# Kernel tuning notes

Hardware: AMD Instinct MI355X
Metric: run time of the kernel (lower is better)

Reference implementation:

```python
import math
import jax
import jax.numpy as jnp
import numpy as np

B = 4
SEQ_LEN = 512
ENC_IN = 21
TIME_DIM = 4
D_MODEL = 256
N_HEADS = 8
HEAD_DIM = D_MODEL // N_HEADS  # 32
NUM_K = 4
PATCH_LEN = 16
STRIDE = 8
EFF_LEN = (SEQ_LEN - PATCH_LEN) // STRIDE + 1  # 63, pad_len == 0
D_FF = 1024
PRED_LEN = 96
N_NEW = 2
N_ENC = 2
EPS = 1e-5


def setup_inputs() -> dict:
    key = jax.random.key(0)
    ks = iter(jax.random.split(key, 100))
    def nrm(shape, s=1.0):
        return jax.random.normal(next(ks), shape, jnp.float32) * s
    H, Dh, T, K = N_HEADS, HEAD_DIM, TIME_DIM, NUM_K
    inp = {}
    inp['x_enc'] = nrm((B, SEQ_LEN, ENC_IN))
    inp['x_mark_enc'] = jax.random.uniform(next(ks), (B, SEQ_LEN, TIME_DIM), jnp.float32)
    inp['x_dec'] = nrm((B, 144, ENC_IN))
    inp['x_mark_dec'] = jax.random.uniform(next(ks), (B, 144, TIME_DIM), jnp.float32)
    # DataEmbedding2: token conv (circular, k=3, no bias); positional enc is computed analytically
    inp['tok_W'] = nrm((D_MODEL, ENC_IN, 3), 0.05)
    # PatchEmbedding conv
    inp['patch_W'] = nrm((D_MODEL, D_MODEL, PATCH_LEN), 0.02)
    inp['patch_b'] = jnp.zeros((D_MODEL,), jnp.float32)
    # TimeKernelAttentionA layers (stacked on leading axis)
    inp['nl_WQ'] = nrm((N_NEW, D_MODEL, D_MODEL), 0.05)
    inp['nl_WK'] = nrm((N_NEW, D_MODEL, D_MODEL), 0.05)
    inp['nl_WV'] = nrm((N_NEW, D_MODEL, D_MODEL), 0.05)
    inp['nl_WO'] = nrm((N_NEW, D_MODEL, D_MODEL), 0.05)
    inp['nl_bO'] = jnp.zeros((N_NEW, D_MODEL), jnp.float32)
    inp['nl_mu_abs'] = nrm((N_NEW, H, Dh, T, K))
    inp['nl_sigma_abs'] = jnp.abs(nrm((N_NEW, H, Dh, T, K))) + 0.5
    inp['nl_w_abs'] = nrm((N_NEW, H, Dh, T, K), 0.1)
    inp['nl_mu_rel'] = nrm((N_NEW, H, Dh, T, K))
    inp['nl_sigma_rel'] = jnp.abs(nrm((N_NEW, H, Dh, T, K))) + 0.5
    inp['nl_w_rel'] = nrm((N_NEW, H, Dh, T, K), 0.1)
    inp['nl_alpha'] = jnp.ones((N_NEW, H), jnp.float32)
    inp['nl_beta'] = jnp.ones((N_NEW, H), jnp.float32)
    inp['nl_gamma'] = jnp.zeros((N_NEW, H), jnp.float32)
    # DataEmbedding_inverted: Linear(EFF_LEN -> d_model)
    inp['inv_W'] = nrm((D_MODEL, EFF_LEN), 0.05)
    inp['inv_b'] = jnp.zeros((D_MODEL,), jnp.float32)
    # Encoder layers (stacked)
    inp['el_Wq'] = nrm((N_ENC, D_MODEL, D_MODEL), 0.05)
    inp['el_bq'] = jnp.zeros((N_ENC, D_MODEL), jnp.float32)
    inp['el_Wk'] = nrm((N_ENC, D_MODEL, D_MODEL), 0.05)
    inp['el_bk'] = jnp.zeros((N_ENC, D_MODEL), jnp.float32)
    inp['el_Wv'] = nrm((N_ENC, D_MODEL, D_MODEL), 0.05)
    inp['el_bv'] = jnp.zeros((N_ENC, D_MODEL), jnp.float32)
    inp['el_Wo'] = nrm((N_ENC, D_MODEL, D_MODEL), 0.05)
    inp['el_bo'] = jnp.zeros((N_ENC, D_MODEL), jnp.float32)
    inp['el_W1'] = nrm((N_ENC, D_FF, D_MODEL), 0.05)
    inp['el_b1'] = jnp.zeros((N_ENC, D_FF), jnp.float32)
    inp['el_W2'] = nrm((N_ENC, D_MODEL, D_FF), 0.05)
    inp['el_b2'] = jnp.zeros((N_ENC, D_MODEL), jnp.float32)
    inp['el_n1_g'] = jnp.ones((N_ENC, D_MODEL), jnp.float32)
    inp['el_n1_b'] = jnp.zeros((N_ENC, D_MODEL), jnp.float32)
    inp['el_n2_g'] = jnp.ones((N_ENC, D_MODEL), jnp.float32)
    inp['el_n2_b'] = jnp.zeros((N_ENC, D_MODEL), jnp.float32)
    inp['norm_g'] = jnp.ones((D_MODEL,), jnp.float32)
    inp['norm_b'] = jnp.zeros((D_MODEL,), jnp.float32)
    inp['proj_W'] = nrm((PRED_LEN, D_MODEL), 0.05)
    inp['proj_b'] = jnp.zeros((PRED_LEN,), jnp.float32)
    return inp


def _conv1d(x, w, stride):
    # x: [B, Cin, L], w: [Cout, Cin, k]
    return jax.lax.conv_general_dilated(x, w, (stride,), 'VALID', dimension_numbers=('NCH', 'OIH', 'NCH'))


def _ln(x, g, b):
    m = x.mean(-1, keepdims=True)
    v = jnp.var(x, axis=-1, keepdims=True)
    return (x - m) / jnp.sqrt(v + EPS) * g + b


def _gauss(t, mu, sigma, w):
    # t: [B, N, T]; mu/sigma/w: [H, D, T, K] -> [B, H, D, N] (sum over T, K)
    diff = t[:, None, None, :, :, None] - mu[None, :, :, None, :, :]
    g = w[None, :, :, None, :, :] * jnp.exp(-(diff * diff) / (2.0 * sigma[None, :, :, None, :, :] ** 2))
    return g.sum((-1, -2))


def _tka(x, t, WQ, WK, WV, WO, bO, mu_a, sg_a, w_a, mu_r, sg_r, w_r, alpha, beta, gamma):
    Bn, L, _ = x.shape
    H, Dh = N_HEADS, HEAD_DIM
    q = (x @ WQ.T).reshape(Bn, L, H, Dh).transpose(0, 2, 1, 3)
    k = (x @ WK.T).reshape(Bn, L, H, Dh).transpose(0, 2, 1, 3)
    v = (x @ WV.T).reshape(Bn, L, H, Dh).transpose(0, 2, 1, 3)
    Xh = x.reshape(Bn, L, H, Dh).transpose(0, 2, 1, 3)
    Pij = jnp.einsum('bhid,bhjd->bhij', Xh, Xh)
    g_abs = _gauss(t, mu_a, sg_a, w_a)  # [B,H,D,L]
    t_rel = jnp.abs(t[:, :, None, :] - t[:, None, :, :]).reshape(Bn, L * L, TIME_DIM)
    g_rel = _gauss(t_rel, mu_r, sg_r, w_r).reshape(Bn, H, Dh, L, L).mean(2)  # [B,H,L,L]
    gi = g_abs.mean(2)  # [B,H,L]
    # NOTE: in the original, g_abs_j = g_abs_i.unsqueeze(-1).expand(...,L) (constant over j),
    # so (g_abs_i.unsqueeze(-1) + g_abs_j) == 2 * g_abs_i broadcast over j. We preserve that.
    a = alpha[None, :, None, None]
    b = beta[None, :, None, None]
    c = gamma[None, :, None, None]
    A = a * Pij * (2.0 * gi[..., None]) + b * Pij * g_rel + c
    scores = jnp.einsum('bhid,bhjd->bhij', q, k) / math.sqrt(Dh) * A
    attn = jax.nn.softmax(scores, axis=-1)
    out = jnp.einsum('bhij,bhjd->bhid', attn, v).transpose(0, 2, 1, 3).reshape(Bn, L, D_MODEL)
    return out @ WO.T + bO


def reference(x_enc, x_mark_enc, x_dec, x_mark_dec, tok_W, patch_W, patch_b, nl_WQ, nl_WK, nl_WV, nl_WO, nl_bO, nl_mu_abs, nl_sigma_abs, nl_w_abs, nl_mu_rel, nl_sigma_rel, nl_w_rel, nl_alpha, nl_beta, nl_gamma, inv_W, inv_b, el_Wq, el_bq, el_Wk, el_bk, el_Wv, el_bv, el_Wo, el_bo, el_W1, el_b1, el_W2, el_b2, el_n1_g, el_n1_b, el_n2_g, el_n2_b, norm_g, norm_b, proj_W, proj_b):
    # --- instance normalization (use_norm) ---
    means = x_enc.mean(1, keepdims=True)
    x = x_enc - means
    stdev = jnp.sqrt(jnp.var(x, axis=1, keepdims=True) + EPS)
    x = x / stdev
    # --- DataEmbedding2: TokenEmbedding (circular conv k=3) + sinusoidal PE, x_mark=None ---
    xc = x.transpose(0, 2, 1)  # [B, C, L]
    xp = jnp.concatenate([xc[:, :, -1:], xc, xc[:, :, :1]], axis=2)  # circular pad 1
    val = _conv1d(xp, tok_W, 1).transpose(0, 2, 1)  # [B, L, d]
    pos = jnp.arange(SEQ_LEN, dtype=jnp.float32)[:, None]
    div = jnp.exp(jnp.arange(0, D_MODEL, 2, dtype=jnp.float32) * (-math.log(10000.0) / D_MODEL))
    pe = jnp.zeros((SEQ_LEN, D_MODEL), jnp.float32)
    pe = pe.at[:, 0::2].set(jnp.sin(pos * div)).at[:, 1::2].set(jnp.cos(pos * div))
    enc = val + pe[None]
    # --- PatchEmbedding (pad_len == 0 for these dims) ---
    enc = _conv1d(enc.transpose(0, 2, 1), patch_W, STRIDE).transpose(0, 2, 1) + patch_b  # [B, 63, d]
    idx = jnp.arange(EFF_LEN)[:, None] * STRIDE + jnp.arange(PATCH_LEN)[None, :]
    t = x_mark_enc[:, idx, :].mean(2)  # [B, 63, T] (unfold + mean)
    # --- TimeKernelAttentionA stack ---
    for i in range(N_NEW):
        enc = _tka(enc, t, nl_WQ[i], nl_WK[i], nl_WV[i], nl_WO[i], nl_bO[i], nl_mu_abs[i], nl_sigma_abs[i], nl_w_abs[i], nl_mu_rel[i], nl_sigma_rel[i], nl_w_rel[i], nl_alpha[i], nl_beta[i], nl_gamma[i])
    # --- DataEmbedding_inverted ---
    xi = jnp.concatenate([enc.transpose(0, 2, 1), t.transpose(0, 2, 1)], axis=1)  # [B, d+T, 63]
    enc = xi @ inv_W.T + inv_b  # [B, d+T, d]
    # --- Encoder (FullAttention + FFN) ---
    Bn, Nt, _ = enc.shape
    for i in range(N_ENC):
        q = (enc @ el_Wq[i].T + el_bq[i]).reshape(Bn, Nt, N_HEADS, HEAD_DIM)
        k = (enc @ el_Wk[i].T + el_bk[i]).reshape(Bn, Nt, N_HEADS, HEAD_DIM)
        v = (enc @ el_Wv[i].T + el_bv[i]).reshape(Bn, Nt, N_HEADS, HEAD_DIM)
        sc = jnp.einsum('blhe,bshe->bhls', q, k) / math.sqrt(HEAD_DIM)
        attn = jax.nn.softmax(sc, axis=-1)
        o = jnp.einsum('bhls,bshd->blhd', attn, v).reshape(Bn, Nt, D_MODEL)
        o = o @ el_Wo[i].T + el_bo[i]
        xn = _ln(enc + o, el_n1_g[i], el_n1_b[i])
        y = jax.nn.gelu(xn @ el_W1[i].T + el_b1[i], approximate=False)
        y = y @ el_W2[i].T + el_b2[i]
        enc = _ln(xn + y, el_n2_g[i], el_n2_b[i])
    enc = _ln(enc, norm_g, norm_b)
    # --- projector + de-normalization ---
    dec = (enc @ proj_W.T + proj_b).transpose(0, 2, 1)[:, :, :ENC_IN]  # [B, pred_len, N]
    dec = dec * stdev[:, 0, :][:, None, :] + means[:, 0, :][:, None, :]
    return dec[:, -PRED_LEN:, :]
```

## Files before the change

### kernel.cpp

```cpp
#include <hip/hip_runtime.h>
#include <hip/hip_bf16.h>

#define NB 4
#define SEQ 512
#define CIN 21
#define TDIM 4
#define DM 256
#define NH 8
#define PLEN 16
#define PSTR 8
#define EL 63
#define DFF 1024
#define PRED 96
#define NT 260
#define EPSV 1e-5f

#define T_nlWQ 0
#define T_nlWK 131072
#define T_nlWV 262144
#define T_nlWO 393216
#define T_elWq 524288
#define T_elWk 655360
#define T_elWv 786432
#define T_elWo 917504
// ... 9 lines not shown
  float s1 = v, s2 = v * v;
  #pragma unroll
  for (int off = 32; off > 0; off >>= 1) {
    s1 += __shfl_down(s1, off, 64);
    s2 += __shfl_down(s2, off, 64);
  }
  int wid = threadIdx.x >> 6, lane = threadIdx.x & 63;
  if (lane == 0) { sb[wid * 2] = s1; sb[wid * 2 + 1] = s2; }
  __syncthreads();
  float m = (sb[0] + sb[2] + sb[4] + sb[6]) * (1.0f / 256.0f);
  float q = (sb[1] + sb[3] + sb[5] + sb[7]) * (1.0f / 256.0f);
  return make_float2(m, q - m * m);
}

__device__ __forceinline__ void load16f(const float* p, float* o) {
  const float4* q = reinterpret_cast<const float4*>(p);
  float4 a = q[0], b = q[1], c = q[2], d = q[3];
  o[0]=a.x; o[1]=a.y; o[2]=a.z; o[3]=a.w;
  o[4]=b.x; o[5]=b.y; o[6]=b.z; o[7]=b.w;
  o[8]=c.x; o[9]=c.y; o[10]=c.z; o[11]=c.w;
  o[12]=d.x; o[13]=d.y; o[14]=d.z; o[15]=d.w;
}

__device__ __forceinline__ float dot32(const float4* a, const float4* b) {
  float s = 0.f;
  #pragma unroll
  for (int i = 0; i < 8; ++i) {
    float4 x = a[i], y = b[i];
    s += x.x*y.x + x.y*y.y + x.z*y.z + x.w*y.w;
  }
  return s;
}

__global__ void __launch_bounds__(256) k_wT(
    const float* __restrict__ nlWQ, const float* __restrict__ nlWK,
    const float* __restrict__ nlWV, const float* __restrict__ nlWO,
    const float* __restrict__ eWq, const float* __restrict__ eWk,
    const float* __restrict__ eWv, const float* __restrict__ eWo,
    const float* __restrict__ eW1, const float* __restrict__ eW2,
    const float* __restrict__ invW, const float* __restrict__ projW,
    const float* __restrict__ tokW, const float* __restrict__ patW,
    float* __restrict__ wt) {
  int blk = blockIdx.x;
  const float* src; float* dst; int R, C, tr, tc;
  if (blk < 1024) {
    int m = blk >> 6, tile = blk & 63;
    tr = tile >> 3; tc = tile & 7; R = 256; C = 256;
    int p = m >> 1, l = m & 1;
    const float* bases[8] = {nlWQ, nlWK, nlWV, nlWO, eWq, eWk, eWv, eWo};
    const int offs[8] = {T_nlWQ, T_nlWK, T_nlWV, T_nlWO, T_elWq, T_elWk, T_elWv, T_elWo};
    src = bases[p] + l * 65536;
    dst = wt + offs[p] + l * 65536;
  } else if (blk < 1536) {
    int q = blk - 1024; int l = q >> 8, s = q & 255;
    tr = s >> 3; tc = s & 7; R = 1024; C = 256;
    src = eW1 + l * 262144; dst = wt + T_elW1 + l * 262144;
  } else if (blk < 2048) {
    int q = blk - 1536; int l = q >> 8, s = q & 255;
    tr = s >> 5; tc = s & 31; R = 256; C = 1024;
    src = eW2 + l * 262144; dst = wt + T_elW2 + l * 262144;
  } else if (blk < 3072) {
    int q = blk - 2048; tr = q >> 7; tc = q & 127; R = 256; C = 4096;
    src = patW; dst = wt + T_pat;
  } else if (blk < 3088) {
    int q = blk - 3072; tr = q >> 1; tc = q & 1; R = 256; C = 63;
    src = invW; dst = wt + T_inv;
  } else if (blk < 3112) {
    int q = blk - 3088; tr = q >> 3; tc = q & 7; R = 96; C = 256;
    src = projW; dst = wt + T_proj;
  } else {
    int q = blk - 3112; tr = q >> 1; tc = q & 1; R = 256; C = 63;
    src = tokW; dst = wt + T_tok;
  }
  __shared__ float ts[32][33];
  int tx = threadIdx.x & 31, ty = threadIdx.x >> 5;
  #pragma unroll
  for (int i = 0; i < 4; ++i) {
    int r = tr * 32 + ty + i * 8, c = tc * 32 + tx;
    ts[ty + i * 8][tx] = (c < C) ? src[(size_t)r * C + c] : 0.f;
  }
  __syncthreads();
  #pragma unroll
  for (int i = 0; i < 4; ++i) {
    int c = tc * 32 + ty + i * 8, r = tr * 32 + tx;
    if (c < C) dst[(size_t)c * R + r] = ts[tx][ty + i * 8];
  }
}

__global__ void k_stats(const float* __restrict__ x, const float* __restrict__ xm,
                        float* __restrict__ means, float* __restrict__ stdev,
                        float* __restrict__ tout) {
  int blk = blockIdx.x;
  int t = threadIdx.x;
  if (blk < NB * CIN) {
    int b = blk / CIN, c = blk % CIN;
    const float* p = x + (size_t)b * SEQ * CIN + c;
    float v0 = p[t * CIN];
    float v1 = p[(t + 256) * CIN];
    float s1 = v0 + v1, s2 = v0 * v0 + v1 * v1;
    __shared__ float sb[8];
    #pragma unroll
    for (int off = 32; off > 0; off >>= 1) {
      s1 += __shfl_down(s1, off, 64);
      s2 += __shfl_down(s2, off, 64);
    }
    int wid = t >> 6, lane = t & 63;
    if (lane == 0) { sb[wid * 2] = s1; sb[wid * 2 + 1] = s2; }
    __syncthreads();
    if (t == 0) {
      float a = sb[0] + sb[2] + sb[4] + sb[6];
      float q = sb[1] + sb[3] + sb[5] + sb[7];
      float m = a * (1.0f / 512.0f);
      float var = q * (1.0f / 512.0f) - m * m;
      means[blk] = m;
      stdev[blk] = sqrtf(var + EPSV);
    }
  } else {
    int idx = (blk - NB * CIN) * 256 + t;
    if (idx >= NB * EL * TDIM) return;
    int b = idx / (EL * TDIM), r = idx % (EL * TDIM);
    int l = r >> 2, ti = r & 3;
    const float* p = xm + (size_t)b * SEQ * TDIM + (size_t)l * PSTR * TDIM + ti;
    float s = 0.f;
    #pragma unroll
    for (int k = 0; k < PLEN; ++k) s += p[k * TDIM];
    tout[idx] = s * (1.f / 16.f);
  }
}

__global__ void __launch_bounds__(256) k_tokconv(
    const float* __restrict__ x, const float* __restrict__ tokWT,
    const float* __restrict__ means, const float* __restrict__ stdev,
    float* __restrict__ enc1) {
  int bi = blockIdx.x;
  int b = bi >> 6, sg = bi & 63;
  int s0 = sg * 8;
  __shared__ float sxr[10 * CIN];
  int t = threadIdx.x;
  if (t < 10 * CIN) {
    int li = t / CIN, c = t % CIN;
    int row = (s0 - 1 + li + SEQ) & 511;
    sxr[t] = (x[(size_t)b * SEQ * CIN + row * CIN + c] - means[b * CIN + c])
             / stdev[b * CIN + c];
  }
  __syncthreads();
  int d = t;
  float wreg[63];
  #pragma unroll
  for (int q = 0; q < 63; ++q) wreg[q] = tokWT[q * DM + d];
  int de = d & ~1;
  float dv = expf((float)de * (-9.210340371976184f / 256.0f));
  bool isodd = (d & 1);
  #pragma unroll 1
  for (int k = 0; k < 8; ++k) {
    float acc = 0.f;
    const float* sr = sxr + k * CIN;
    #pragma unroll
    for (int c = 0; c < CIN; ++c) {
      acc += sr[c]           * wreg[c * 3 + 0];
// ... 167 lines not shown
    for (int q = 0; q < 4; ++q)
      #pragma unroll
      for (int r = 0; r < 8; ++r) {
        float xv = xb[r * DM + k0 + q];
        acc[r][0] += xv * w[q].x; acc[r][1] += xv * w[q].y;
        acc[r][2] += xv * w[q].z; acc[r][3] += xv * w[q].w;
      }
  }
  if (kq) {
    #pragma unroll
    for (int r = 0; r < 8; ++r)
      reinterpret_cast<float4*>(sp)[((kq - 1) * 8 + r) * 64 + colg] =
          make_float4(acc[r][0], acc[r][1], acc[r][2], acc[r][3]);
  }
  __syncthreads();
  if (kq == 0) {
    float4 b4 = reinterpret_cast<const float4*>(bias)[colg];
    const float4* sp4 = reinterpret_cast<const float4*>(sp);
    #pragma unroll
    for (int r = 0; r < 8; ++r) {
      float4 p0 = sp4[(0 * 8 + r) * 64 + colg];
      float4 p1 = sp4[(1 * 8 + r) * 64 + colg];
      float4 p2 = sp4[(2 * 8 + r) * 64 + colg];
      float4 o;
      o.x = acc[r][0] + p0.x + p1.x + p2.x + b4.x;
      o.y = acc[r][1] + p0.y + p1.y + p2.y + b4.y;
      o.z = acc[r][2] + p0.z + p1.z + p2.z + b4.z;
      o.w = acc[r][3] + p0.w + p1.w + p2.w + b4.w;
      reinterpret_cast<float4*>(out + (size_t)(row0 + r) * DM)[colg] = o;
    }
  }
}

__global__ void __launch_bounds__(256) k_grel2(
    const float* __restrict__ tws,
    const float* __restrict__ mu_r, const float* __restrict__ sg_r,
    const float* __restrict__ w_r,
    const float* __restrict__ mu_a, const float* __restrict__ sg_a,
    const float* __restrict__ w_a,
    float* __restrict__ grel, float* __restrict__ gib) {
  int blk = blockIdx.x;
  int L = blk / (NB * 252);
  int rem0 = blk % (NB * 252);
  int b = rem0 / 252, chunk = rem0 % 252;
  int po = L * 4096;
  float* grelL = grel + (size_t)L * (NB * NH * EL * EL);
  float* gibL  = gib + (size_t)L * (NB * NH * EL);
  int t = threadIdx.x;
  int h = t >> 5, dh = t & 31;
  __shared__ float s_t[EL * TDIM];
  if (t < EL * TDIM) s_t[t] = tws[b * EL * TDIM + t];
  float pm[16], pc[16], pw[16];
  load16f(mu_r + po + (size_t)t * 16, pm);
  load16f(sg_r + po + (size_t)t * 16, pc);
  load16f(w_r  + po + (size_t)t * 16, pw);
  #pragma unroll
  for (int p = 0; p < 16; ++p) pc[p] = -0.5f / (pc[p] * pc[p]);
  __syncthreads();
  #pragma unroll 1
  for (int q = 0; q < 8; ++q) {
    int p = chunk * 8 + q;
    int i = (int)((127.0f - sqrtf(16129.0f - 8.0f * (float)p)) * 0.5f);
    while (i * (127 - i) / 2 > p) --i;
    while ((i + 1) * (126 - i) / 2 <= p) ++i;
    int j = i + (p - i * (127 - i) / 2);
    float dvv[4];
    dvv[0] = fabsf(s_t[i*4+0] - s_t[j*4+0]);
    dvv[1] = fabsf(s_t[i*4+1] - s_t[j*4+1]);
    dvv[2] = fabsf(s_t[i*4+2] - s_t[j*4+2]);
    dvv[3] = fabsf(s_t[i*4+3] - s_t[j*4+3]);
    float srel = 0.f;
    #pragma unroll
    for (int tt = 0; tt < 4; ++tt)
      #pragma unroll
      for (int k = 0; k < 4; ++k) {
        int pp = tt * 4 + k;
        float df = dvv[tt] - pm[pp];
        srel += pw[pp] * __expf(pc[pp] * df * df);
      }
    #pragma unroll
    for (int m = 1; m < 32; m <<= 1) srel += __shfl_xor(srel, m, 64);
    if (dh == 0) {
      float v = srel * (1.f / 32.f);
      grelL[(((size_t)b * NH + h) * EL + i) * EL + j] = v;
      grelL[(((size_t)b * NH + h) * EL + j) * EL + i] = v;
    }
  }
  if (chunk < EL) {
    load16f(mu_a + po + (size_t)t * 16, pm);
    load16f(sg_a + po + (size_t)t * 16, pc);
    load16f(w_a  + po + (size_t)t * 16, pw);
    #pragma unroll
    for (int p = 0; p < 16; ++p) pc[p] = -0.5f / (pc[p] * pc[p]);
    int i = chunk;
    float tiv[4] = {s_t[i*4+0], s_t[i*4+1], s_t[i*4+2], s_t[i*4+3]};
    float sabs = 0.f;
    #pragma unroll
    for (int tt = 0; tt < 4; ++tt)
      #pragma unroll
      for (int k = 0; k < 4; ++k) {
        int pp = tt * 4 + k;
        float df = tiv[tt] - pm[pp];
        sabs += pw[pp] * __expf(pc[pp] * df * df);
      }
    #pragma unroll
    for (int m = 1; m < 32; m <<= 1) sabs += __shfl_xor(sabs, m, 64);
    if (dh == 0) gibL[((size_t)b * NH + h) * EL + i] = sabs * (1.f / 32.f);
  }
}

__global__ void __launch_bounds__(512) k_tka_attn_f(
    const float* __restrict__ xin, const float* __restrict__ qw,
    const float* __restrict__ kw, const float* __restrict__ vw,
    const float* __restrict__ grel, const float* __restrict__ gib,
    const float* __restrict__ alpha, const float* __restrict__ beta,
    const float* __restrict__ gamma,
    const float* __restrict__ WOT, const float* __restrict__ bO,
    float* __restrict__ xout) {
  int bi = blockIdx.x;
  int b = bi / EL, i = bi % EL;
  int t = threadIdx.x;
  __shared__ __align__(16) float sQX[2 * DM];
  __shared__ float sP[NH * 64];
  __shared__ __align__(16) float sO[DM];
  __shared__ float sPV[DM];
  if (t < 2 * DM)
    sQX[t] = (t < DM) ? qw[(size_t)bi * DM + t] : xin[(size_t)bi * DM + (t - DM)];
  __syncthreads();
  {
    int tile = t >> 8, h = (t >> 5) & 7, jj = t & 31;
    int j = tile * 32 + jj;
    bool valid = (j < EL);
    int jc = valid ? j : (EL - 1);
    float gi = gib[((size_t)b * NH + h) * EL + i];
    float al = alpha[h], be = beta[h], ga = gamma[h];
    const float* grow = grel + (((size_t)b * NH + h) * EL + i) * EL;
    const float4* kp = reinterpret_cast<const float4*>(
        kw + (size_t)(b * EL + jc) * DM + h * 32);
    const float4* xp = reinterpret_cast<const float4*>(
        xin + (size_t)(b * EL + jc) * DM + h * 32);
    float4 kf[8], xf[8];
    #pragma unroll
    for (int q = 0; q < 8; ++q) { kf[q] = kp[q]; xf[q] = xp[q]; }
// ... 197 lines not shown
    __syncthreads();
    float ov[4] = {0.f, 0.f, 0.f, 0.f};
    float gg = g[col], bb2 = bb[col];
    if (!kh) {
      float bias = bo[col];
      #pragma unroll
      for (int r = 0; r < 4; ++r)
        ov[r] = acc[r] + sPV[r * DM + col] + bias
              + resin[((size_t)(b * NT + i0 + r)) * DM + col];
    }
    int wid = t >> 6, lane = t & 63;
    #pragma unroll 1
    for (int r = 0; r < 4; ++r) {
      float o = (!kh) ? ov[r] : 0.f;
      __syncthreads();
      float s1 = o, s2 = o * o;
      #pragma unroll
      for (int off = 32; off > 0; off >>= 1) {
        s1 += __shfl_down(s1, off, 64);
        s2 += __shfl_down(s2, off, 64);
      }
      if (lane == 0 && wid < 4) { sb[wid * 2] = s1; sb[wid * 2 + 1] = s2; }
      __syncthreads();
      float m = (sb[0] + sb[2] + sb[4] + sb[6]) * (1.f / 256.f);
      float q2 = (sb[1] + sb[3] + sb[5] + sb[7]) * (1.f / 256.f);
      float var = q2 - m * m;
      if (!kh)
        out[((size_t)(b * NT + i0 + r)) * DM + col] =
            (ov[r] - m) * rsqrtf(var + EPSV) * gg + bb2;
    }
  }
}

__global__ void __launch_bounds__(256) k_ffn1(
    const float* __restrict__ W1T, const float* __restrict__ b1,
    const float* __restrict__ xn, float* __restrict__ y1, int gpb) {
  int bi = blockIdx.x;
  int rg = bi >> 2, fg = bi & 3;
  int row0 = gpb ? ((rg / gpb) * NT + (rg % gpb) * 8) : rg * 8;
  __shared__ __align__(16) float sx[8 * DM];
  __shared__ __align__(16) float sp[3 * 8 * DM];
  int t = threadIdx.x;
  int colg = t & 63, kq = t >> 6;
  #pragma unroll
  for (int i = 0; i < 2; ++i)
    reinterpret_cast<float4*>(sx)[t + i * 256] =
        reinterpret_cast<const float4*>(xn + (size_t)row0 * DM)[t + i * 256];
  __syncthreads();
  int f = fg * 256 + colg * 4;
  float acc[8][4];
  #pragma unroll
  for (int r = 0; r < 8; ++r) { acc[r][0]=0.f; acc[r][1]=0.f; acc[r][2]=0.f; acc[r][3]=0.f; }
  const float* xb = sx + kq * 64;
  const float4* wp = reinterpret_cast<const float4*>(W1T + (size_t)(kq * 64) * DFF + f);
  #pragma unroll 1
  for (int k0 = 0; k0 < 64; k0 += 4) {
    float4 w[4];
    #pragma unroll
    for (int q = 0; q < 4; ++q) w[q] = wp[(size_t)(k0 + q) * 256];
    #pragma unroll
    for (int q = 0; q < 4; ++q)
      #pragma unroll
      for (int r = 0; r < 8; ++r) {
        float xv = xb[r * DM + k0 + q];
        acc[r][0] += xv * w[q].x; acc[r][1] += xv * w[q].y;
        acc[r][2] += xv * w[q].z; acc[r][3] += xv * w[q].w;
      }
  }
  if (kq) {
    #pragma unroll
    for (int r = 0; r < 8; ++r)
      reinterpret_cast<float4*>(sp)[((kq - 1) * 8 + r) * 64 + colg] =
          make_float4(acc[r][0], acc[r][1], acc[r][2], acc[r][3]);
  }
  __syncthreads();
  if (kq == 0) {
    float4 b4 = *reinterpret_cast<const float4*>(b1 + f);
    const float4* sp4 = reinterpret_cast<const float4*>(sp);
    #pragma unroll 1
    for (int r = 0; r < 8; ++r) {
      float4 p0 = sp4[(0 * 8 + r) * 64 + colg];
      float4 p1 = sp4[(1 * 8 + r) * 64 + colg];
      float4 p2 = sp4[(2 * 8 + r) * 64 + colg];
      float a0 = acc[r][0] + p0.x + p1.x + p2.x + b4.x;
      float a1 = acc[r][1] + p0.y + p1.y + p2.y + b4.y;
      float a2 = acc[r][2] + p0.z + p1.z + p2.z + b4.z;
      float a3 = acc[r][3] + p0.w + p1.w + p2.w + b4.w;
      float4 o;
      o.x = 0.5f * a0 * (1.f + erff(a0 * 0.70710678118654752f));
      o.y = 0.5f * a1 * (1.f + erff(a1 * 0.70710678118654752f));
      o.z = 0.5f * a2 * (1.f + erff(a2 * 0.70710678118654752f));
      o.w = 0.5f * a3 * (1.f + erff(a3 * 0.70710678118654752f));
      *reinterpret_cast<float4*>(y1 + (size_t)(row0 + r) * DFF + f) = o;
    }
  }
}

__global__ void __launch_bounds__(256) k_ffn2f(
    const float* __restrict__ W2T, const float* __restrict__ b2,
    const float* __restrict__ g, const float* __restrict__ bb,
    const float* __restrict__ y1, const float* __restrict__ xn,
    float* __restrict__ out, int gpb) {
  int blk = blockIdx.x;
  int row0 = gpb ? ((blk / gpb) * NT + (blk % gpb) * 4) : blk * 4;
  __shared__ __align__(16) float sy[4 * DFF];
  __shared__ __align__(16) float sp[3 * 4 * DM];
  int t = threadIdx.x;
  int colg = t & 63, kq = t >> 6;
  #pragma unroll
  for (int i = 0; i < 4; ++i)
    reinterpret_cast<float4*>(sy)[t + i * 256] =
        reinterpret_cast<const float4*>(y1 + (size_t)row0 * DFF)[t + i * 256];
  __syncthreads();
  float acc[4][4];
  #pragma unroll
  for (int r = 0; r < 4; ++r) { acc[r][0]=0.f; acc[r][1]=0.f; acc[r][2]=0.f; acc[r][3]=0.f; }
  const float* yb = sy + kq * 256;
  const float4* wp = reinterpret_cast<const float4*>(W2T + (size_t)(kq * 256) * DM) + colg;
  #pragma unroll 1
  for (int k0 = 0; k0 < 256; k0 += 8) {
    float4 w[8];
    #pragma unroll
    for (int q = 0; q < 8; ++q) w[q] = wp[(size_t)(k0 + q) * 64];
    #pragma unroll
    for (int q = 0; q < 8; ++q)
      #pragma unroll
      for (int r = 0; r < 4; ++r) {
        float yv = yb[r * DFF + k0 + q];
        acc[r][0] += yv * w[q].x; acc[r][1] += yv * w[q].y;
        acc[r][2] += yv * w[q].z; acc[r][3] += yv * w[q].w;
      }
  }
  if (kq) {
    #pragma unroll
    for (int r = 0; r < 4; ++r)
      reinterpret_cast<float4*>(sp)[((kq - 1) * 4 + r) * 64 + colg] =
          make_float4(acc[r][0], acc[r][1], acc[r][2], acc[r][3]);
  }
  __syncthreads();
  if (kq == 0) {
    float4 b4 = reinterpret_cast<const float4*>(b2)[colg];
    float4 g4 = reinterpret_cast<const float4*>(g)[colg];
    float4 bb4 = reinterpret_cast<const float4*>(bb)[colg];
    const float4* sp4 = reinterpret_cast<const float4*>(sp);
    #pragma unroll 1
    for (int r = 0; r < 4; ++r) {
      float4 p0 = sp4[(0 * 4 + r) * 64 + colg];
      float4 p1 = sp4[(1 * 4 + r) * 64 + colg];
      float4 p2 = sp4[(2 * 4 + r) * 64 + colg];
      float4 xr = reinterpret_cast<const float4*>(xn + (size_t)(row0 + r) * DM)[colg];
      float o0 = acc[r][0] + p0.x + p1.x + p2.x + b4.x + xr.x;
      float o1 = acc[r][1] + p0.y + p1.y + p2.y + b4.y + xr.y;
      float o2 = acc[r][2] + p0.z + p1.z + p2.z + b4.z + xr.z;
      float o3 = acc[r][3] + p0.w + p1.w + p2.w + b4.w + xr.w;
      float s1 = o0 + o1 + o2 + o3;
      float s2 = o0*o0 + o1*o1 + o2*o2 + o3*o3;
      #pragma unroll
      for (int m = 1; m < 64; m <<= 1) {
        s1 += __shfl_xor(s1, m, 64);
        s2 += __shfl_xor(s2, m, 64);
      }
      float mean = s1 * (1.f / 256.f);
      float var = s2 * (1.f / 256.f) - mean * mean;
      float rs = rsqrtf(var + EPSV);
      float4 o;
      o.x = (o0 - mean) * rs * g4.x + bb4.x;
      o.y = (o1 - mean) * rs * g4.y + bb4.y;
      o.z = (o2 - mean) * rs * g4.z + bb4.z;
      o.w = (o3 - mean) * rs * g4.w + bb4.w;
      reinterpret_cast<float4*>(out + (size_t)(row0 + r) * DM)[colg] = o;
    }
  }
}

__global__ void k_final(const float* __restrict__ g, const float* __restrict__ bb,
                        const float* __restrict__ pWT, const float* __restrict__ pb,
                        const float* __restrict__ enc2,
                        const float* __restrict__ stdev, const float* __restrict__ means,
                        float* __restrict__ out) {
  int bi = blockIdx.x;
  int b = bi / CIN, c = bi % CIN;
  __shared__ __align__(16) float sx[DM];
  __shared__ float sb[8];
// ... 43 lines not shown
  const float* inv_b   = (const float*)d_in[22];
  const float* el_Wq   = (const float*)d_in[23];
  const float* el_bq   = (const float*)d_in[24];
  const float* el_Wk   = (const float*)d_in[25];
  const float* el_bk   = (const float*)d_in[26];
  const float* el_Wv   = (const float*)d_in[27];
  const float* el_bv   = (const float*)d_in[28];
  const float* el_Wo   = (const float*)d_in[29];
  const float* el_bo   = (const float*)d_in[30];
  const float* el_W1   = (const float*)d_in[31];
  const float* el_b1   = (const float*)d_in[32];
  const float* el_W2   = (const float*)d_in[33];
  const float* el_b2   = (const float*)d_in[34];
  const float* n1g     = (const float*)d_in[35];
  const float* n1b     = (const float*)d_in[36];
  const float* n2g     = (const float*)d_in[37];
  const float* n2b     = (const float*)d_in[38];
  const float* norm_g  = (const float*)d_in[39];
  const float* norm_b  = (const float*)d_in[40];
  const float* proj_W  = (const float*)d_in[41];
  const float* proj_b  = (const float*)d_in[42];

  float* ws = (float*)d_ws;
  float* means = ws + 0;
  float* stdev = ws + 96;
  float* tws   = ws + 192;
  float* enc1  = ws + 1216;
  float* encP  = ws + 525504;
  float* pbuf  = ws + 590016;
  float* enc2  = ws + 1106112;
  float* qb    = ws + 1638592;
  float* kb    = ws + 1904832;
  float* vb    = ws + 2171072;
  float* y1    = ws + 2437312;
  float* encPb = ws + 3502272;
  float* grel  = ws + 4567232;
  float* gib   = ws + 4821248;
  float* wsT   = ws + 4825344;
  float* xn    = qb;

  k_wT<<<3128, 256, 0, stream>>>(nl_WQ, nl_WK, nl_WV, nl_WO,
                                 el_Wq, el_Wk, el_Wv, el_Wo,
                                 el_W1, el_W2, inv_W, proj_W,
                                 tok_W, patch_W, wsT);
  k_stats<<<NB * CIN + 4, 256, 0, stream>>>(x_enc, x_mark, means, stdev, tws);
  k_grel2<<<2 * NB * 252, 256, 0, stream>>>(tws, nl_mu_r, nl_sg_r, nl_w_r,
                                            nl_mu_a, nl_sg_a, nl_w_a, grel, gib);
  k_tokconv<<<NB * 64, 256, 0, stream>>>(x_enc, wsT + T_tok, means, stdev, enc1);
  k_patch_part<<<42 * 8, 256, 0, stream>>>(enc1, wsT + T_pat, pbuf);
  k_patch_red<<<NB * EL, 256, 0, stream>>>(pbuf, patch_b, encP);

  for (int L = 0; L < 2; ++L) {
    size_t wo = (size_t)L * DM * DM;
    const float* xi = L ? encPb : encP;
    float* xo       = L ? encP : encPb;
    k_qkv2<4><<<63 * 3, 256, 0, stream>>>(wsT + T_nlWQ + wo, wsT + T_nlWK + wo,
                                          wsT + T_nlWV + wo,
                                          nullptr, nullptr, nullptr,
                                          xi, qb, kb, vb);
    k_tka_attn_f<<<NB * EL, 512, 0, stream>>>(xi, qb, kb, vb,
        grel + (size_t)L * (NB * NH * EL * EL), gib + (size_t)L * (NB * NH * EL),
        nl_al + L * 8, nl_be + L * 8, nl_ga + L * 8,
        wsT + T_nlWO + wo, nl_bO + L * DM, xo);
  }

  k_invemb<<<NB * NT, 256, 0, stream>>>(wsT + T_inv, inv_b, encP, tws, enc2);

  k_qkv2<8><<<130 * 3, 256, 0, stream>>>(wsT + T_elWq, wsT + T_elWk, wsT + T_elWv,
                                         el_bq, el_bk, el_bv,
                                         enc2, qb, kb, vb);
  k_enc_attn_f<<<NB * 65, 512, 0, stream>>>(qb, kb, vb, wsT + T_elWo, el_bo,
                                            n1g, n1b, enc2, xn, 65);
  k_ffn1<<<130 * 4, 256, 0, stream>>>(wsT + T_elW1, el_b1, xn, y1, 0);
  k_ffn2f<<<260, 256, 0, stream>>>(wsT + T_elW2, el_b2, n2g, n2b, y1, xn, enc2, 0);

  {
    size_t wo = (size_t)DM * DM;
    size_t bo = (size_t)DM;
    size_t fo = (size_t)DFF * DM;
    k_qkv_l1<<<272, 256, 0, stream>>>(wsT + T_elWq + wo, wsT + T_elWk + wo,
                                      wsT + T_elWv + wo,
                                      el_bq + bo, el_bk + bo, el_bv + bo,
                                      enc2, qb, kb, vb);
    k_enc_attn_f<<<NB * 6, 512, 0, stream>>>(qb, kb, vb, wsT + T_elWo + wo,
                                             el_bo + bo, n1g + bo, n1b + bo,
                                             enc2, xn, 6);
    k_ffn1<<<12 * 4, 256, 0, stream>>>(wsT + T_elW1 + fo, el_b1 + DFF, xn, y1, 3);
    k_ffn2f<<<NB * 6, 256, 0, stream>>>(wsT + T_elW2 + fo, el_b2 + bo,
                                        n2g + bo, n2b + bo, y1, xn, enc2, 6);
  }

  k_final<<<NB * CIN, 256, 0, stream>>>(norm_g, norm_b, wsT + T_proj, proj_b,
                                        enc2, stdev, means, (float*)d_out);
}
```

Before: 444.4 us.

## Merge prep kernels into one launch and fuse FFN1 into FFN2

The weight transpose, stats, and Gaussian-kernel precompute kernels are merged into a single launch. The grel path now recomputes the patch-averaged time features itself, so it no longer depends on the stats output. FFN1 with GELU is folded into the FFN2+LayerNorm kernel: the intermediate stays in shared memory and the y1 round trip through global memory goes away. In exchange, the fused FFN uses fewer blocks (260 vs 520+260), and each block streams the full W1, which lowers parallelism.

```diff
diff --git a/kernel.cpp b/kernel.cpp
--- a/kernel.cpp
+++ b/kernel.cpp
@@ -65,7 +65,7 @@
   return s;
 }
 
-__global__ void __launch_bounds__(256) k_wT(
+__global__ void __launch_bounds__(256) k_prep(
     const float* __restrict__ nlWQ, const float* __restrict__ nlWK,
     const float* __restrict__ nlWV, const float* __restrict__ nlWO,
     const float* __restrict__ eWq, const float* __restrict__ eWk,
@@ -73,91 +73,174 @@
     const float* __restrict__ eW1, const float* __restrict__ eW2,
     const float* __restrict__ invW, const float* __restrict__ projW,
     const float* __restrict__ tokW, const float* __restrict__ patW,
-    float* __restrict__ wt) {
-  int blk = blockIdx.x;
-  const float* src; float* dst; int R, C, tr, tc;
-  if (blk < 1024) {
-    int m = blk >> 6, tile = blk & 63;
-    tr = tile >> 3; tc = tile & 7; R = 256; C = 256;
-    int p = m >> 1, l = m & 1;
-    const float* bases[8] = {nlWQ, nlWK, nlWV, nlWO, eWq, eWk, eWv, eWo};
-    const int offs[8] = {T_nlWQ, T_nlWK, T_nlWV, T_nlWO, T_elWq, T_elWk, T_elWv, T_elWo};
-    src = bases[p] + l * 65536;
-    dst = wt + offs[p] + l * 65536;
-  } else if (blk < 1536) {
-    int q = blk - 1024; int l = q >> 8, s = q & 255;
-    tr = s >> 3; tc = s & 7; R = 1024; C = 256;
-    src = eW1 + l * 262144; dst = wt + T_elW1 + l * 262144;
-  } else if (blk < 2048) {
-    int q = blk - 1536; int l = q >> 8, s = q & 255;
-    tr = s >> 5; tc = s & 31; R = 256; C = 1024;
-    src = eW2 + l * 262144; dst = wt + T_elW2 + l * 262144;
-  } else if (blk < 3072) {
-    int q = blk - 2048; tr = q >> 7; tc = q & 127; R = 256; C = 4096;
-    src = patW; dst = wt + T_pat;
-  } else if (blk < 3088) {
-    int q = blk - 3072; tr = q >> 1; tc = q & 1; R = 256; C = 63;
-    src = invW; dst = wt + T_inv;
-  } else if (blk < 3112) {
-    int q = blk - 3088; tr = q >> 3; tc = q & 7; R = 96; C = 256;
-    src = projW; dst = wt + T_proj;
-  } else {
-    int q = blk - 3112; tr = q >> 1; tc = q & 1; R = 256; C = 63;
-    src = tokW; dst = wt + T_tok;
-  }
-  __shared__ float ts[32][33];
-  int tx = threadIdx.x & 31, ty = threadIdx.x >> 5;
-  #pragma unroll
-  for (int i = 0; i < 4; ++i) {
-    int r = tr * 32 + ty + i * 8, c = tc * 32 + tx;
-    ts[ty + i * 8][tx] = (c < C) ? src[(size_t)r * C + c] : 0.f;
-  }
-  __syncthreads();
-  #pragma unroll
-  for (int i = 0; i < 4; ++i) {
-    int c = tc * 32 + ty + i * 8, r = tr * 32 + tx;
-    if (c < C) dst[(size_t)c * R + r] = ts[tx][ty + i * 8];
-  }
-}
-
-__global__ void k_stats(const float* __restrict__ x, const float* __restrict__ xm,
-                        float* __restrict__ means, float* __restrict__ stdev,
-                        float* __restrict__ tout) {
+    float* __restrict__ wt,
+    const float* __restrict__ x, const float* __restrict__ xm,
+    float* __restrict__ means, float* __restrict__ stdev,
+    float* __restrict__ tout,
+    const float* __restrict__ mu_r, const float* __restrict__ sg_r,
+    const float* __restrict__ w_r,
+    const float* __restrict__ mu_a, const float* __restrict__ sg_a,
+    const float* __restrict__ w_a,
+    float* __restrict__ grel, float* __restrict__ gib) {
+  __shared__ float smem[32 * 33];
   int blk = blockIdx.x;
   int t = threadIdx.x;
-  if (blk < NB * CIN) {
-    int b = blk / CIN, c = blk % CIN;
-    const float* p = x + (size_t)b * SEQ * CIN + c;
-    float v0 = p[t * CIN];
-    float v1 = p[(t + 256) * CIN];
-    float s1 = v0 + v1, s2 = v0 * v0 + v1 * v1;
-    __shared__ float sb[8];
-    #pragma unroll
-    for (int off = 32; off > 0; off >>= 1) {
-      s1 += __shfl_down(s1, off, 64);
-      s2 += __shfl_down(s2, off, 64);
-    }
-    int wid = t >> 6, lane = t & 63;
-    if (lane == 0) { sb[wid * 2] = s1; sb[wid * 2 + 1] = s2; }
+
+  if (blk < 3128) {
+    const float* src; float* dst; int R, C, tr, tc;
+    if (blk < 1024) {
+      int m = blk >> 6, tile = blk & 63;
+      tr = tile >> 3; tc = tile & 7; R = 256; C = 256;
+      int p = m >> 1, l = m & 1;
+      const float* bases[8] = {nlWQ, nlWK, nlWV, nlWO, eWq, eWk, eWv, eWo};
+      const int offs[8] = {T_nlWQ, T_nlWK, T_nlWV, T_nlWO, T_elWq, T_elWk, T_elWv, T_elWo};
+      src = bases[p] + l * 65536;
+      dst = wt + offs[p] + l * 65536;
+    } else if (blk < 1536) {
+      int q = blk - 1024; int l = q >> 8, s = q & 255;
+      tr = s >> 3; tc = s & 7; R = 1024; C = 256;
+      src = eW1 + l * 262144; dst = wt + T_elW1 + l * 262144;
+    } else if (blk < 2048) {
+      int q = blk - 1536; int l = q >> 8, s = q & 255;
+      tr = s >> 5; tc = s & 31; R = 256; C = 1024;
+      src = eW2 + l * 262144; dst = wt + T_elW2 + l * 262144;
+    } else if (blk < 3072) {
+      int q = blk - 2048; tr = q >> 7; tc = q & 127; R = 256; C = 4096;
+      src = patW; dst = wt + T_pat;
+    } else if (blk < 3088) {
+      int q = blk - 3072; tr = q >> 1; tc = q & 1; R = 256; C = 63;
+      src = invW; dst = wt + T_inv;
+    } else if (blk < 3112) {
+      int q = blk - 3088; tr = q >> 3; tc = q & 7; R = 96; C = 256;
+      src = projW; dst = wt + T_proj;
+    } else {
+      int q = blk - 3112; tr = q >> 1; tc = q & 1; R = 256; C = 63;
+      src = tokW; dst = wt + T_tok;
+    }
+    float (*ts)[33] = (float(*)[33])smem;
+    int tx = t & 31, ty = t >> 5;
+    #pragma unroll
+    for (int i = 0; i < 4; ++i) {
+      int r = tr * 32 + ty + i * 8, c = tc * 32 + tx;
+      ts[ty + i * 8][tx] = (c < C) ? src[(size_t)r * C + c] : 0.f;
+    }
     __syncthreads();
-    if (t == 0) {
-      float a = sb[0] + sb[2] + sb[4] + sb[6];
-      float q = sb[1] + sb[3] + sb[5] + sb[7];
-      float m = a * (1.0f / 512.0f);
-      float var = q * (1.0f / 512.0f) - m * m;
-      means[blk] = m;
-      stdev[blk] = sqrtf(var + EPSV);
+    #pragma unroll
+    for (int i = 0; i < 4; ++i) {
+      int c = tc * 32 + ty + i * 8, r = tr * 32 + tx;
+      if (c < C) dst[(size_t)c * R + r] = ts[tx][ty + i * 8];
+    }
+  } else if (blk < 3216) {
+    int sblk = blk - 3128;
+    if (sblk < NB * CIN) {
+      int b = sblk / CIN, c = sblk % CIN;
+      const float* p = x + (size_t)b * SEQ * CIN + c;
+      float v0 = p[t * CIN];
+      float v1 = p[(t + 256) * CIN];
+      float s1 = v0 + v1, s2 = v0 * v0 + v1 * v1;
+      float* sb = smem;
+      #pragma unroll
+      for (int off = 32; off > 0; off >>= 1) {
+        s1 += __shfl_down(s1, off, 64);
+        s2 += __shfl_down(s2, off, 64);
+      }
+      int wid = t >> 6, lane = t & 63;
+      if (lane == 0) { sb[wid * 2] = s1; sb[wid * 2 + 1] = s2; }
+      __syncthreads();
+      if (t == 0) {
+        float a = sb[0] + sb[2] + sb[4] + sb[6];
+        float q = sb[1] + sb[3] + sb[5] + sb[7];
+        float m = a * (1.0f / 512.0f);
+        float var = q * (1.0f / 512.0f) - m * m;
+        means[sblk] = m;
+        stdev[sblk] = sqrtf(var + EPSV);
+      }
+    } else {
+      int idx = (sblk - NB * CIN) * 256 + t;
+      if (idx >= NB * EL * TDIM) return;
+      int b = idx / (EL * TDIM), r = idx % (EL * TDIM);
+      int l = r >> 2, ti = r & 3;
+      const float* p = xm + (size_t)b * SEQ * TDIM + (size_t)l * PSTR * TDIM + ti;
+      float s = 0.f;
+      #pragma unroll
+      for (int k = 0; k < PLEN; ++k) s += p[k * TDIM];
+      tout[idx] = s * (1.f / 16.f);
     }
   } else {
-    int idx = (blk - NB * CIN) * 256 + t;
-    if (idx >= NB * EL * TDIM) return;
-    int b = idx / (EL * TDIM), r = idx % (EL * TDIM);
-    int l = r >> 2, ti = r & 3;
-    const float* p = xm + (size_t)b * SEQ * TDIM + (size_t)l * PSTR * TDIM + ti;
-    float s = 0.f;
-    #pragma unroll
-    for (int k = 0; k < PLEN; ++k) s += p[k * TDIM];
-    tout[idx] = s * (1.f / 16.f);
+    int gblk = blk - 3216;
+    int L = gblk / (NB * 252);
+    int rem0 = gblk % (NB * 252);
+    int b = rem0 / 252, chunk = rem0 % 252;
+    int po = L * 4096;
+    float* grelL = grel + (size_t)L * (NB * NH * EL * EL);
+    float* gibL  = gib + (size_t)L * (NB * NH * EL);
+    int h = t >> 5, dh = t & 31;
+    float* s_t = smem;
+    if (t < EL * TDIM) {
+      int l = t >> 2, ti = t & 3;
+      const float* p = xm + (size_t)b * SEQ * TDIM + (size_t)l * PSTR * TDIM + ti;
+      float s = 0.f;
+      #pragma unroll
+      for (int k = 0; k < PLEN; ++k) s += p[k * TDIM];
+      s_t[t] = s * (1.f / 16.f);
+    }
+    float pm[16], pc[16], pw[16];
+    load16f(mu_r + po + (size_t)t * 16, pm);
+    load16f(sg_r + po + (size_t)t * 16, pc);
+    load16f(w_r  + po + (size_t)t * 16, pw);
+    #pragma unroll
+    for (int p = 0; p < 16; ++p) pc[p] = -0.5f / (pc[p] * pc[p]);
+    __syncthreads();
+    #pragma unroll 1
+    for (int q = 0; q < 8; ++q) {
+      int p = chunk * 8 + q;
+      int i = (int)((127.0f - sqrtf(16129.0f - 8.0f * (float)p)) * 0.5f);
+      while (i * (127 - i) / 2 > p) --i;
+      while ((i + 1) * (126 - i) / 2 <= p) ++i;
+      int j = i + (p - i * (127 - i) / 2);
+      float dvv[4];
+      dvv[0] = fabsf(s_t[i*4+0] - s_t[j*4+0]);
+      dvv[1] = fabsf(s_t[i*4+1] - s_t[j*4+1]);
+      dvv[2] = fabsf(s_t[i*4+2] - s_t[j*4+2]);
+      dvv[3] = fabsf(s_t[i*4+3] - s_t[j*4+3]);
+      float srel = 0.f;
+      #pragma unroll
+      for (int tt = 0; tt < 4; ++tt)
+        #pragma unroll
+        for (int k = 0; k < 4; ++k) {
+          int pp = tt * 4 + k;
+          float df = dvv[tt] - pm[pp];
+          srel += pw[pp] * __expf(pc[pp] * df * df);
+        }
+      #pragma unroll
+      for (int m = 1; m < 32; m <<= 1) srel += __shfl_xor(srel, m, 64);
+      if (dh == 0) {
+        float v = srel * (1.f / 32.f);
+        grelL[(((size_t)b * NH + h) * EL + i) * EL + j] = v;
+        grelL[(((size_t)b * NH + h) * EL + j) * EL + i] = v;
+      }
+    }
+    if (chunk < EL) {
+      load16f(mu_a + po + (size_t)t * 16, pm);
+      load16f(sg_a + po + (size_t)t * 16, pc);
+      load16f(w_a  + po + (size_t)t * 16, pw);
+      #pragma unroll
+      for (int p = 0; p < 16; ++p) pc[p] = -0.5f / (pc[p] * pc[p]);
+      int i = chunk;
+      float tiv[4] = {s_t[i*4+0], s_t[i*4+1], s_t[i*4+2], s_t[i*4+3]};
+      float sabs = 0.f;
+      #pragma unroll
+      for (int tt = 0; tt < 4; ++tt)
+        #pragma unroll
+        for (int k = 0; k < 4; ++k) {
+          int pp = tt * 4 + k;
+          float df = tiv[tt] - pm[pp];
+          sabs += pw[pp] * __expf(pc[pp] * df * df);
+        }
+      #pragma unroll
+      for (int m = 1; m < 32; m <<= 1) sabs += __shfl_xor(sabs, m, 64);
+      if (dh == 0) gibL[((size_t)b * NH + h) * EL + i] = sabs * (1.f / 32.f);
+    }
   }
 }
 
@@ -391,83 +474,6 @@
   }
 }
 
-__global__ void __launch_bounds__(256) k_grel2(
-    const float* __restrict__ tws,
-    const float* __restrict__ mu_r, const float* __restrict__ sg_r,
-    const float* __restrict__ w_r,
-    const float* __restrict__ mu_a, const float* __restrict__ sg_a,
-    const float* __restrict__ w_a,
-    float* __restrict__ grel, float* __restrict__ gib) {
-  int blk = blockIdx.x;
-  int L = blk / (NB * 252);
-  int rem0 = blk % (NB * 252);
-  int b = rem0 / 252, chunk = rem0 % 252;
-  int po = L * 4096;
-  float* grelL = grel + (size_t)L * (NB * NH * EL * EL);
-  float* gibL  = gib + (size_t)L * (NB * NH * EL);
-  int t = threadIdx.x;
-  int h = t >> 5, dh = t & 31;
-  __shared__ float s_t[EL * TDIM];
-  if (t < EL * TDIM) s_t[t] = tws[b * EL * TDIM + t];
-  float pm[16], pc[16], pw[16];
-  load16f(mu_r + po + (size_t)t * 16, pm);
-  load16f(sg_r + po + (size_t)t * 16, pc);
-  load16f(w_r  + po + (size_t)t * 16, pw);
-  #pragma unroll
-  for (int p = 0; p < 16; ++p) pc[p] = -0.5f / (pc[p] * pc[p]);
-  __syncthreads();
-  #pragma unroll 1
-  for (int q = 0; q < 8; ++q) {
-    int p = chunk * 8 + q;
-    int i = (int)((127.0f - sqrtf(16129.0f - 8.0f * (float)p)) * 0.5f);
-    while (i * (127 - i) / 2 > p) --i;
-    while ((i + 1) * (126 - i) / 2 <= p) ++i;
-    int j = i + (p - i * (127 - i) / 2);
-    float dvv[4];
-    dvv[0] = fabsf(s_t[i*4+0] - s_t[j*4+0]);
-    dvv[1] = fabsf(s_t[i*4+1] - s_t[j*4+1]);
-    dvv[2] = fabsf(s_t[i*4+2] - s_t[j*4+2]);
-    dvv[3] = fabsf(s_t[i*4+3] - s_t[j*4+3]);
-    float srel = 0.f;
-    #pragma unroll
-    for (int tt = 0; tt < 4; ++tt)
-      #pragma unroll
-      for (int k = 0; k < 4; ++k) {
-        int pp = tt * 4 + k;
-        float df = dvv[tt] - pm[pp];
-        srel += pw[pp] * __expf(pc[pp] * df * df);
-      }
-    #pragma unroll
-    for (int m = 1; m < 32; m <<= 1) srel += __shfl_xor(srel, m, 64);
-    if (dh == 0) {
-      float v = srel * (1.f / 32.f);
-      grelL[(((size_t)b * NH + h) * EL + i) * EL + j] = v;
-      grelL[(((size_t)b * NH + h) * EL + j) * EL + i] = v;
-    }
-  }
-  if (chunk < EL) {
-    load16f(mu_a + po + (size_t)t * 16, pm);
-    load16f(sg_a + po + (size_t)t * 16, pc);
-    load16f(w_a  + po + (size_t)t * 16, pw);
-    #pragma unroll
-    for (int p = 0; p < 16; ++p) pc[p] = -0.5f / (pc[p] * pc[p]);
-    int i = chunk;
-    float tiv[4] = {s_t[i*4+0], s_t[i*4+1], s_t[i*4+2], s_t[i*4+3]};
-    float sabs = 0.f;
-    #pragma unroll
-    for (int tt = 0; tt < 4; ++tt)
-      #pragma unroll
-      for (int k = 0; k < 4; ++k) {
-        int pp = tt * 4 + k;
-        float df = tiv[tt] - pm[pp];
-        sabs += pw[pp] * __expf(pc[pp] * df * df);
-      }
-    #pragma unroll
-    for (int m = 1; m < 32; m <<= 1) sabs += __shfl_xor(sabs, m, 64);
-    if (dh == 0) gibL[((size_t)b * NH + h) * EL + i] = sabs * (1.f / 32.f);
-  }
-}
-
 __global__ void __launch_bounds__(512) k_tka_attn_f(
     const float* __restrict__ xin, const float* __restrict__ qw,
     const float* __restrict__ kw, const float* __restrict__ vw,
@@ -731,86 +737,74 @@
   }
 }
 
-__global__ void __launch_bounds__(256) k_ffn1(
+__global__ void __launch_bounds__(256) k_ffnf(
     const float* __restrict__ W1T, const float* __restrict__ b1,
-    const float* __restrict__ xn, float* __restrict__ y1, int gpb) {
-  int bi = blockIdx.x;
-  int rg = bi >> 2, fg = bi & 3;
-  int row0 = gpb ? ((rg / gpb) * NT + (rg % gpb) * 8) : rg * 8;
-  __shared__ __align__(16) float sx[8 * DM];
-  __shared__ __align__(16) float sp[3 * 8 * DM];
-  int t = threadIdx.x;
-  int colg = t & 63, kq = t >> 6;
-  #pragma unroll
-  for (int i = 0; i < 2; ++i)
-    reinterpret_cast<float4*>(sx)[t + i * 256] =
-        reinterpret_cast<const float4*>(xn + (size_t)row0 * DM)[t + i * 256];
-  __syncthreads();
-  int f = fg * 256 + colg * 4;
-  float acc[8][4];
-  #pragma unroll
-  for (int r = 0; r < 8; ++r) { acc[r][0]=0.f; acc[r][1]=0.f; acc[r][2]=0.f; acc[r][3]=0.f; }
-  const float* xb = sx + kq * 64;
-  const float4* wp = reinterpret_cast<const float4*>(W1T + (size_t)(kq * 64) * DFF + f);
-  #pragma unroll 1
-  for (int k0 = 0; k0 < 64; k0 += 4) {
-    float4 w[4];
-    #pragma unroll
-    for (int q = 0; q < 4; ++q) w[q] = wp[(size_t)(k0 + q) * 256];
-    #pragma unroll
-    for (int q = 0; q < 4; ++q)
-      #pragma unroll
-      for (int r = 0; r < 8; ++r) {
-        float xv = xb[r * DM + k0 + q];
-        acc[r][0] += xv * w[q].x; acc[r][1] += xv * w[q].y;
-        acc[r][2] += xv * w[q].z; acc[r][3] += xv * w[q].w;
-      }
-  }
-  if (kq) {
-    #pragma unroll
-    for (int r = 0; r < 8; ++r)
-      reinterpret_cast<float4*>(sp)[((kq - 1) * 8 + r) * 64 + colg] =
-          make_float4(acc[r][0], acc[r][1], acc[r][2], acc[r][3]);
-  }
-  __syncthreads();
-  if (kq == 0) {
-    float4 b4 = *reinterpret_cast<const float4*>(b1 + f);
-    const float4* sp4 = reinterpret_cast<const float4*>(sp);
-    #pragma unroll 1
-    for (int r = 0; r < 8; ++r) {
-      float4 p0 = sp4[(0 * 8 + r) * 64 + colg];
-      float4 p1 = sp4[(1 * 8 + r) * 64 + colg];
-      float4 p2 = sp4[(2 * 8 + r) * 64 + colg];
-      float a0 = acc[r][0] + p0.x + p1.x + p2.x + b4.x;
-      float a1 = acc[r][1] + p0.y + p1.y + p2.y + b4.y;
-      float a2 = acc[r][2] + p0.z + p1.z + p2.z + b4.z;
-      float a3 = acc[r][3] + p0.w + p1.w + p2.w + b4.w;
-      float4 o;
-      o.x = 0.5f * a0 * (1.f + erff(a0 * 0.70710678118654752f));
-      o.y = 0.5f * a1 * (1.f + erff(a1 * 0.70710678118654752f));
-      o.z = 0.5f * a2 * (1.f + erff(a2 * 0.70710678118654752f));
-      o.w = 0.5f * a3 * (1.f + erff(a3 * 0.70710678118654752f));
-      *reinterpret_cast<float4*>(y1 + (size_t)(row0 + r) * DFF + f) = o;
-    }
-  }
-}
-
-__global__ void __launch_bounds__(256) k_ffn2f(
     const float* __restrict__ W2T, const float* __restrict__ b2,
     const float* __restrict__ g, const float* __restrict__ bb,
-    const float* __restrict__ y1, const float* __restrict__ xn,
-    float* __restrict__ out, int gpb) {
+    const float* __restrict__ xn, float* __restrict__ out, int gpb) {
   int blk = blockIdx.x;
   int row0 = gpb ? ((blk / gpb) * NT + (blk % gpb) * 4) : blk * 4;
+  __shared__ __align__(16) float sx[4 * DM];
   __shared__ __align__(16) float sy[4 * DFF];
   __shared__ __align__(16) float sp[3 * 4 * DM];
   int t = threadIdx.x;
   int colg = t & 63, kq = t >> 6;
-  #pragma unroll
-  for (int i = 0; i < 4; ++i)
-    reinterpret_cast<float4*>(sy)[t + i * 256] =
-        reinterpret_cast<const float4*>(y1 + (size_t)row0 * DFF)[t + i * 256];
-  __syncthreads();
+  reinterpret_cast<float4*>(sx)[t] =
+      reinterpret_cast<const float4*>(xn + (size_t)row0 * DM)[t];
+  __syncthreads();
+
+  #pragma unroll 1
+  for (int fg = 0; fg < 4; ++fg) {
+    float acc[4][4];
+    #pragma unroll
+    for (int r = 0; r < 4; ++r) { acc[r][0]=0.f; acc[r][1]=0.f; acc[r][2]=0.f; acc[r][3]=0.f; }
+    const float* xb = sx + kq * 64;
+    const float4* wp = reinterpret_cast<const float4*>(W1T + (size_t)(kq * 64) * DFF)
+                       + (fg * 64 + colg);
+    #pragma unroll 1
+    for (int k0 = 0; k0 < 64; k0 += 4) {
+      float4 w[4];
+      #pragma unroll
+      for (int q = 0; q < 4; ++q) w[q] = wp[(size_t)(k0 + q) * 256];
+      #pragma unroll
+      for (int q = 0; q < 4; ++q)
+        #pragma unroll
+        for (int r = 0; r < 4; ++r) {
+          float xv = xb[r * DM + k0 + q];
+          acc[r][0] += xv * w[q].x; acc[r][1] += xv * w[q].y;
+          acc[r][2] += xv * w[q].z; acc[r][3] += xv * w[q].w;
+        }
+    }
+    if (kq) {
+      #pragma unroll
+      for (int r = 0; r < 4; ++r)
+        reinterpret_cast<float4*>(sp)[((kq - 1) * 4 + r) * 64 + colg] =
+            make_float4(acc[r][0], acc[r][1], acc[r][2], acc[r][3]);
+    }
+    __syncthreads();
+    if (kq == 0) {
+      float4 b4 = *reinterpret_cast<const float4*>(b1 + fg * 256 + colg * 4);
+      const float4* sp4 = reinterpret_cast<const float4*>(sp);
+      #pragma unroll
+      for (int r = 0; r < 4; ++r) {
+        float4 p0 = sp4[(0 * 4 + r) * 64 + colg];
+        float4 p1 = sp4[(1 * 4 + r) * 64 + colg];
+        float4 p2 = sp4[(2 * 4 + r) * 64 + colg];
+        float a0 = acc[r][0] + p0.x + p1.x + p2.x + b4.x;
+        float a1 = acc[r][1] + p0.y + p1.y + p2.y + b4.y;
+        float a2 = acc[r][2] + p0.z + p1.z + p2.z + b4.z;
+        float a3 = acc[r][3] + p0.w + p1.w + p2.w + b4.w;
+        float4 o;
+        o.x = 0.5f * a0 * (1.f + erff(a0 * 0.70710678118654752f));
+        o.y = 0.5f * a1 * (1.f + erff(a1 * 0.70710678118654752f));
+        o.z = 0.5f * a2 * (1.f + erff(a2 * 0.70710678118654752f));
+        o.w = 0.5f * a3 * (1.f + erff(a3 * 0.70710678118654752f));
+        reinterpret_cast<float4*>(sy)[r * 256 + fg * 64 + colg] = o;
+      }
+    }
+    __syncthreads();
+  }
+
   float acc[4][4];
   #pragma unroll
   for (int r = 0; r < 4; ++r) { acc[r][0]=0.f; acc[r][1]=0.f; acc[r][2]=0.f; acc[r][3]=0.f; }
@@ -847,7 +841,7 @@
       float4 p0 = sp4[(0 * 4 + r) * 64 + colg];
       float4 p1 = sp4[(1 * 4 + r) * 64 + colg];
       float4 p2 = sp4[(2 * 4 + r) * 64 + colg];
-      float4 xr = reinterpret_cast<const float4*>(xn + (size_t)(row0 + r) * DM)[colg];
+      float4 xr = reinterpret_cast<const float4*>(sx)[r * 64 + colg];
       float o0 = acc[r][0] + p0.x + p1.x + p2.x + b4.x + xr.x;
       float o1 = acc[r][1] + p0.y + p1.y + p2.y + b4.y + xr.y;
       float o2 = acc[r][2] + p0.z + p1.z + p2.z + b4.z + xr.z;
@@ -957,20 +951,19 @@
   float* qb    = ws + 1638592;
   float* kb    = ws + 1904832;
   float* vb    = ws + 2171072;
-  float* y1    = ws + 2437312;
   float* encPb = ws + 3502272;
   float* grel  = ws + 4567232;
   float* gib   = ws + 4821248;
   float* wsT   = ws + 4825344;
   float* xn    = qb;
 
-  k_wT<<<3128, 256, 0, stream>>>(nl_WQ, nl_WK, nl_WV, nl_WO,
-                                 el_Wq, el_Wk, el_Wv, el_Wo,
-                                 el_W1, el_W2, inv_W, proj_W,
-                                 tok_W, patch_W, wsT);
-  k_stats<<<NB * CIN + 4, 256, 0, stream>>>(x_enc, x_mark, means, stdev, tws);
-  k_grel2<<<2 * NB * 252, 256, 0, stream>>>(tws, nl_mu_r, nl_sg_r, nl_w_r,
-                                            nl_mu_a, nl_sg_a, nl_w_a, grel, gib);
+  k_prep<<<5232, 256, 0, stream>>>(nl_WQ, nl_WK, nl_WV, nl_WO,
+                                   el_Wq, el_Wk, el_Wv, el_Wo,
+                                   el_W1, el_W2, inv_W, proj_W,
+                                   tok_W, patch_W, wsT,
+                                   x_enc, x_mark, means, stdev, tws,
+                                   nl_mu_r, nl_sg_r, nl_w_r,
+                                   nl_mu_a, nl_sg_a, nl_w_a, grel, gib);
   k_tokconv<<<NB * 64, 256, 0, stream>>>(x_enc, wsT + T_tok, means, stdev, enc1);
   k_patch_part<<<42 * 8, 256, 0, stream>>>(enc1, wsT + T_pat, pbuf);
   k_patch_red<<<NB * EL, 256, 0, stream>>>(pbuf, patch_b, encP);
@@ -996,8 +989,8 @@
                                          enc2, qb, kb, vb);
   k_enc_attn_f<<<NB * 65, 512, 0, stream>>>(qb, kb, vb, wsT + T_elWo, el_bo,
                                             n1g, n1b, enc2, xn, 65);
-  k_ffn1<<<130 * 4, 256, 0, stream>>>(wsT + T_elW1, el_b1, xn, y1, 0);
-  k_ffn2f<<<260, 256, 0, stream>>>(wsT + T_elW2, el_b2, n2g, n2b, y1, xn, enc2, 0);
+  k_ffnf<<<260, 256, 0, stream>>>(wsT + T_elW1, el_b1, wsT + T_elW2, el_b2,
+                                  n2g, n2b, xn, enc2, 0);
 
   {
     size_t wo = (size_t)DM * DM;
@@ -1010,9 +1003,9 @@
     k_enc_attn_f<<<NB * 6, 512, 0, stream>>>(qb, kb, vb, wsT + T_elWo + wo,
                                              el_bo + bo, n1g + bo, n1b + bo,
                                              enc2, xn, 6);
-    k_ffn1<<<12 * 4, 256, 0, stream>>>(wsT + T_elW1 + fo, el_b1 + DFF, xn, y1, 3);
-    k_ffn2f<<<NB * 6, 256, 0, stream>>>(wsT + T_elW2 + fo, el_b2 + bo,
-                                        n2g + bo, n2b + bo, y1, xn, enc2, 6);
+    k_ffnf<<<NB * 6, 256, 0, stream>>>(wsT + T_elW1 + fo, el_b1 + DFF,
+                                       wsT + T_elW2 + fo, el_b2 + bo,
+                                       n2g + bo, n2b + bo, xn, enc2, 6);
   }
 
   k_final<<<NB * CIN, 256, 0, stream>>>(norm_g, norm_b, wsT + T_proj, proj_b,
```

After: 467.6 us. 5.2% more time.
